# Kernel tuning notes

Hardware: AMD Instinct MI355X
Metric: run time of the kernel (lower is better)

## Reference

```python
import jax, jax.numpy as jnp
import numpy as np

N = 4096   # query tokens
M = 4096   # key/value tokens
D = 512    # embedding_dim


def setup_inputs() -> dict:
    key = jax.random.key(0)
    kq, kk, kv = jax.random.split(key, 3)
    return {
        "query": jax.random.normal(kq, (N, D), dtype=jnp.float32),
        "key": jax.random.normal(kk, (M, D), dtype=jnp.float32),
        "value": jax.random.normal(kv, (M, D), dtype=jnp.float32),
    }


def reference(query, key, value):
    # scores = Q K^T  (no 1/sqrt(d) scaling in the original module)
    attention_scores = jnp.einsum("nd,md->nm", query, key)  # [N, M]
    attention_probs = jax.nn.softmax(attention_scores, axis=-1)  # [N, M]
    output = jnp.einsum("nm,md->nd", attention_probs, value)  # [N, D]
    return (output, attention_probs)
```

## Files before the change

kernel.cpp:

```cpp
#include <hip/hip_runtime.h>
#include <hip/hip_bf16.h>
#include <stdint.h>

#define N_Q 4096
#define N_K 4096
#define DIM 512

typedef float f32x4 __attribute__((ext_vector_type(4)));
typedef __bf16 bf16x8 __attribute__((ext_vector_type(8)));
typedef unsigned short u16x4 __attribute__((ext_vector_type(4)));

__device__ __forceinline__ f32x4 mfma_bf16(bf16x8 a, bf16x8 b, f32x4 c) {
  return __builtin_amdgcn_mfma_f32_16x16x32_bf16(a, b, c, 0, 0, 0);
}

__device__ __forceinline__ void gload16(const void* g, void* l) {
  __builtin_amdgcn_global_load_lds((const __attribute__((address_space(1))) void*)g,
                                   (__attribute__((address_space(3))) void*)l,
                                   16, 0, 0);
}

__device__ __forceinline__ void split4(const f32x4 v, u16x4& h, u16x4& l) {
#pragma unroll
  for (int i = 0; i < 4; ++i) {
    float f = v[i];
    uint32_t u = __builtin_bit_cast(uint32_t, f);
    uint32_t hb = (u + 0x8000u) & 0xffff0000u;
    float hf = __builtin_bit_cast(float, hb);
    float lf = f - hf;
    h[i] = (unsigned short)(hb >> 16);
    l[i] = (unsigned short)(__builtin_bit_cast(uint32_t, lf) >> 16);
  }
}

__device__ __forceinline__ unsigned short bf16r(float f) {
  uint32_t u = __builtin_bit_cast(uint32_t, f);
  return (unsigned short)((u + 0x8000u) >> 16);
}

__global__ __launch_bounds__(256, 2) void qk_kernel(const float* __restrict__ Q,
                                                    const float* __restrict__ K,
                                                    float* __restrict__ S) {
  __shared__ __align__(16) char sAh[16384];
  __shared__ __align__(16) char sAl[16384];
  __shared__ __align__(16) char sBh[16384];
  __shared__ __align__(16) char sBl[16384];

  const int tid = threadIdx.x;
  const int rbase = blockIdx.y * 128;
  const int cbase = blockIdx.x * 128;
  const int lane = tid & 63, wid = tid >> 6;
  const int wr = wid >> 1, wc = wid & 1;
  const int lr = lane & 15, lk = (lane >> 4) * 8;

  const int srow = tid >> 4;
  const int scol = (tid & 15) * 4;

  f32x4 qr[8], kr[8];
#pragma unroll
  for (int p = 0; p < 8; ++p) {
    int r = p * 16 + srow;
    qr[p] = *(const f32x4*)(Q + (size_t)(rbase + r) * DIM + scol);
    kr[p] = *(const f32x4*)(K + (size_t)(cbase + r) * DIM + scol);
  }

  const f32x4 fzero = {0.f, 0.f, 0.f, 0.f};
  f32x4 acc[4][4];
#pragma unroll
  for (int m = 0; m < 4; ++m)
#pragma unroll
    for (int n = 0; n < 4; ++n) acc[m][n] = fzero;

  for (int kk = 0; kk < DIM / 64; ++kk) {
    __syncthreads();
#pragma unroll
    for (int p = 0; p < 8; ++p) {
      int r = p * 16 + srow;
      uint32_t bo = (uint32_t)(r * 128) + (uint32_t)((scol * 2) ^ ((r & 7) << 4));
      u16x4 qh, ql, kh, kl;
      split4(qr[p], qh, ql);
      split4(kr[p], kh, kl);
      *(u16x4*)(sAh + bo) = qh;
      *(u16x4*)(sAl + bo) = ql;
      *(u16x4*)(sBh + bo) = kh;
      *(u16x4*)(sBl + bo) = kl;
    }
    __syncthreads();
    if (kk < DIM / 64 - 1) {
#pragma unroll
      for (int p = 0; p < 8; ++p) {
        int r = p * 16 + srow;
        qr[p] = *(const f32x4*)(Q + (size_t)(rbase + r) * DIM + (kk + 1) * 64 + scol);
        kr[p] = *(const f32x4*)(K + (size_t)(cbase + r) * DIM + (kk + 1) * 64 + scol);
      }
    }
#pragma unroll
    for (int kh = 0; kh < 2; ++kh) {
      bf16x8 a_h[4], a_l[4], b_h[4], b_l[4];
#pragma unroll
      for (int m = 0; m < 4; ++m) {
        int row = wr * 64 + m * 16 + lr;
        uint32_t co = (uint32_t)(((kh * 32 + lk) * 2) ^ ((row & 7) << 4));
        a_h[m] = *(const bf16x8*)(sAh + row * 128 + co);
        a_l[m] = *(const bf16x8*)(sAl + row * 128 + co);
      }
#pragma unroll
      for (int n = 0; n < 4; ++n) {
        int row = wc * 64 + n * 16 + lr;
        uint32_t co = (uint32_t)(((kh * 32 + lk) * 2) ^ ((row & 7) << 4));
        b_h[n] = *(const bf16x8*)(sBh + row * 128 + co);
        b_l[n] = *(const bf16x8*)(sBl + row * 128 + co);
      }
#pragma unroll
      for (int m = 0; m < 4; ++m)
#pragma unroll
        for (int n = 0; n < 4; ++n) {
          acc[m][n] = mfma_bf16(a_h[m], b_h[n], acc[m][n]);
          acc[m][n] = mfma_bf16(a_h[m], b_l[n], acc[m][n]);
          acc[m][n] = mfma_bf16(a_l[m], b_h[n], acc[m][n]);
        }
    }
  }

#pragma unroll
  for (int m = 0; m < 4; ++m) {
    int row = rbase + wr * 64 + m * 16 + (lane >> 4) * 4;
#pragma unroll
    for (int n = 0; n < 4; ++n) {
      int col = cbase + wc * 64 + n * 16 + lr;
#pragma unroll
      for (int j = 0; j < 4; ++j)
        S[(size_t)(row + j) * N_K + col] = acc[m][n][j];
    }
  }
}

__global__ __launch_bounds__(256) void softmax_kernel(float* __restrict__ P,
                                                      unsigned short* __restrict__ Pb) {
  const int tid = threadIdx.x;
  const int wid = tid >> 6, lane = tid & 63;
  float* p = P + (size_t)blockIdx.x * N_K;

  f32x4 v[4];
  float mx = -3.0e38f;
#pragma unroll
  for (int i = 0; i < 4; ++i) {
    v[i] = *(const f32x4*)(p + i * 1024 + tid * 4);
    mx = fmaxf(mx, fmaxf(fmaxf(v[i][0], v[i][1]), fmaxf(v[i][2], v[i][3])));
  }
#pragma unroll
  for (int o = 32; o > 0; o >>= 1) mx = fmaxf(mx, __shfl_xor(mx, o, 64));
  __shared__ float redM[4];
  __shared__ float redS[4];
  if (lane == 0) redM[wid] = mx;
  __syncthreads();
  mx = fmaxf(fmaxf(redM[0], redM[1]), fmaxf(redM[2], redM[3]));

  float s = 0.f;
#pragma unroll
  for (int i = 0; i < 4; ++i) {
#pragma unroll
    for (int j = 0; j < 4; ++j) {
      v[i][j] = __expf(v[i][j] - mx);
      s += v[i][j];
    }
  }
#pragma unroll
  for (int o = 32; o > 0; o >>= 1) s += __shfl_xor(s, o, 64);
  if (lane == 0) redS[wid] = s;
  __syncthreads();
  s = redS[0] + redS[1] + redS[2] + redS[3];
  const float inv = 1.0f / s;

  unsigned short* pb = Pb ? (Pb + (size_t)blockIdx.x * N_K) : nullptr;
#pragma unroll
  for (int i = 0; i < 4; ++i) {
    v[i] *= inv;
    *(f32x4*)(p + i * 1024 + tid * 4) = v[i];
    if (pb) {
      u16x4 h;
#pragma unroll
      for (int j = 0; j < 4; ++j) h[j] = bf16r(v[i][j]);
      *(u16x4*)(pb + i * 1024 + tid * 4) = h;
    }
  }
}

__global__ __launch_bounds__(256) void vt_kernel(const float* __restrict__ V,
                                                 unsigned short* __restrict__ Vt) {
  __shared__ unsigned short t[64][72];
  const int tid = threadIdx.x;
  const int d0 = blockIdx.x * 64;
  const int k0 = blockIdx.y * 64;

#pragma unroll
  for (int c = 0; c < 4; ++c) {
    int kr = (tid >> 4) + c * 16;
    f32x4 v = *(const f32x4*)(V + (size_t)(k0 + kr) * DIM + d0 + (tid & 15) * 4);
#pragma unroll
    for (int j = 0; j < 4; ++j) t[(tid & 15) * 4 + j][kr] = bf16r(v[j]);
  }
  __syncthreads();
#pragma unroll
  for (int c = 0; c < 2; ++c) {
    int d = (tid >> 3) + c * 32;
    int k = (tid & 7) * 8;
    *(uint4*)(Vt + (size_t)(d0 + d) * N_K + k0 + k) = *(const uint4*)&t[d][k];
  }
}

__global__ __launch_bounds__(256, 2) void pv3_kernel(const unsigned short* __restrict__ Pb,
                                                     const unsigned short* __restrict__ Vt,
                                                     float* __restrict__ Opart,
                                                     int kspan) {
  __shared__ __align__(16) char smem[65536];

  const int tid = threadIdx.x;
  const int lane = tid & 63, wid = tid >> 6;
  const int wr = wid >> 1, wc = wid & 1;
  const int rbase = blockIdx.y * 128;
  const int cbase = blockIdx.x * 128;
  const int k0 = blockIdx.z * kspan;
  float* Out = Opart + (size_t)blockIdx.z * ((size_t)N_Q * DIM);

  const int lrow = lane >> 3;
  const int lchk = lane & 7;
  const int iters = kspan >> 6;

  const f32x4 fzero = {0.f, 0.f, 0.f, 0.f};
  f32x4 acc[4][4];
#pragma unroll
  for (int m = 0; m < 4; ++m)
#pragma unroll
    for (int n = 0; n < 4; ++n) acc[m][n] = fzero;

  auto stage = [&](int buf, int t) {
    const size_t kel = (size_t)k0 + ((size_t)t << 6);
#pragma unroll
    for (int i = 0; i < 4; ++i) {
      const int rr = (wid << 5) + (i << 3) + lrow;
      const int gc = lchk ^ (rr & 7);
      const void* gA = (const void*)(Pb + (size_t)(rbase + rr) * N_K + kel + (gc << 3));
      uint32_t off = (uint32_t)(buf * 32768 + (((wid << 5) + (i << 3)) << 7));
      off = (uint32_t)__builtin_amdgcn_readfirstlane((int)off);
      gload16(gA, smem + off);
    }
#pragma unroll
    for (int i = 0; i < 4; ++i) {
      const int rr = (wid << 5) + (i << 3) + lrow;
      const int gc = lchk ^ (rr & 7);
      const void* gB = (const void*)(Vt + (size_t)(cbase + rr) * N_K + kel + (gc << 3));
      uint32_t off = (uint32_t)(buf * 32768 + 16384 + (((wid << 5) + (i << 3)) << 7));
      off = (uint32_t)__builtin_amdgcn_readfirstlane((int)off);
      gload16(gB, smem + off);
    }
  };

  auto compute = [&](int buf) {
    const char* bA = smem + buf * 32768;
    const char* bB = bA + 16384;
#pragma unroll
    for (int kh = 0; kh < 2; ++kh) {
      bf16x8 a[4], b[4];
#pragma unroll
      for (int m = 0; m < 4; ++m) {
        int row = (wr << 6) + (m << 4) + (lane & 15);
        uint32_t co = (uint32_t)(((((kh << 2) + (lane >> 4)) << 4)) ^ ((row & 7) << 4));
        a[m] = *(const bf16x8*)(bA + row * 128 + co);
      }
#pragma unroll
      for (int n = 0; n < 4; ++n) {
        int row = (wc << 6) + (n << 4) + (lane & 15);
        uint32_t co = (uint32_t)(((((kh << 2) + (lane >> 4)) << 4)) ^ ((row & 7) << 4));
        b[n] = *(const bf16x8*)(bB + row * 128 + co);
      }
#pragma unroll
      for (int m = 0; m < 4; ++m)
#pragma unroll
        for (int n = 0; n < 4; ++n)
          acc[m][n] = mfma_bf16(a[m], b[n], acc[m][n]);
    }
  };

  stage(0, 0);
  __syncthreads();
  int cur = 0;
  for (int t = 0; t < iters; ++t) {
    if (t + 1 < iters) stage(cur ^ 1, t + 1);
    compute(cur);
    __syncthreads();
    cur ^= 1;
  }

#pragma unroll
  for (int m = 0; m < 4; ++m) {
    int row = rbase + wr * 64 + m * 16 + (lane >> 4) * 4;
#pragma unroll
    for (int n = 0; n < 4; ++n) {
      int col = cbase + wc * 64 + n * 16 + (lane & 15);
#pragma unroll
      for (int j = 0; j < 4; ++j)
        Out[(size_t)(row + j) * DIM + col] = acc[m][n][j];
    }
  }
}

__global__ __launch_bounds__(256) void reduce_kernel(float* __restrict__ O,
                                                     const float* __restrict__ Opart,
                                                     int nsplit) {
  size_t i = ((size_t)blockIdx.x * 256 + threadIdx.x) * 4;
  f32x4 s = *(const f32x4*)(Opart + i);
  for (int z = 1; z < nsplit; ++z)
    s += *(const f32x4*)(Opart + (size_t)z * ((size_t)N_Q * DIM) + i);
  *(f32x4*)(O + i) = s;
}

__global__ __launch_bounds__(512, 2) void pv_kernel(const float* __restrict__ P,
                                                    const float* __restrict__ V,
                                                    float* __restrict__ O) {
  __shared__ __align__(16) char sA[16384];
  __shared__ __align__(16) char sB[16384];

  const int tid = threadIdx.x;
  const int rbase = blockIdx.y * 128;
  const int cbase = blockIdx.x * 128;
  const int lane = tid & 63, wid = tid >> 6;
  const int wr = wid >> 2, wc = wid & 3;
  const int lr = lane & 15, lk = (lane >> 4) * 8;

  const int a_row = tid >> 4;
  const int a_col = (tid & 15) * 4;
  const int b_c = tid & 127;
  const int b_oct = tid >> 7;

  f32x4 areg[4];
  float breg[4][4];
#pragma unroll
  for (int p = 0; p < 4; ++p) {
    int r = p * 32 + a_row;
    areg[p] = *(const f32x4*)(P + (size_t)(rbase + r) * N_K + a_col);
  }
#pragma unroll
  for (int g = 0; g < 4; ++g) {
    int kr0 = b_oct * 4 + g * 16;
#pragma unroll
    for (int i = 0; i < 4; ++i)
      breg[g][i] = V[(size_t)(kr0 + i) * DIM + cbase + b_c];
  }

  const f32x4 fzero = {0.f, 0.f, 0.f, 0.f};
  f32x4 acc[4][2];
#pragma unroll
  for (int m = 0; m < 4; ++m)
#pragma unroll
    for (int n = 0; n < 2; ++n) acc[m][n] = fzero;

  for (int kk = 0; kk < N_K / 64; ++kk) {
    __syncthreads();
#pragma unroll
    for (int p = 0; p < 4; ++p) {
      int r = p * 32 + a_row;
      uint32_t bo = (uint32_t)(r * 128) + (uint32_t)((a_col * 2) ^ ((r & 7) << 4));
      u16x4 hv;
#pragma unroll
      for (int i = 0; i < 4; ++i) hv[i] = bf16r(areg[p][i]);
      *(u16x4*)(sA + bo) = hv;
    }
#pragma unroll
    for (int g = 0; g < 4; ++g) {
      int kr0 = b_oct * 4 + g * 16;
      uint32_t bo = (uint32_t)(b_c * 128) + (uint32_t)((kr0 * 2) ^ ((b_c & 7) << 4));
      u16x4 hv;
#pragma unroll
      for (int i = 0; i < 4; ++i) hv[i] = bf16r(breg[g][i]);
      *(u16x4*)(sB + bo) = hv;
    }
    __syncthreads();
    if (kk < N_K / 64 - 1) {
#pragma unroll
      for (int p = 0; p < 4; ++p) {
        int r = p * 32 + a_row;
        areg[p] = *(const f32x4*)(P + (size_t)(rbase + r) * N_K + (kk + 1) * 64 + a_col);
      }
#pragma unroll
      for (int g = 0; g < 4; ++g) {
        int kr0 = b_oct * 4 + g * 16;
#pragma unroll
        for (int i = 0; i < 4; ++i)
          breg[g][i] = V[(size_t)((kk + 1) * 64 + kr0 + i) * DIM + cbase + b_c];
      }
    }
#pragma unroll
    for (int kh = 0; kh < 2; ++kh) {
      bf16x8 af[4], bf[2];
#pragma unroll
      for (int m = 0; m < 4; ++m) {
        int row = wr * 64 + m * 16 + lr;
        uint32_t co = (uint32_t)(((kh * 32 + lk) * 2) ^ ((row & 7) << 4));
        af[m] = *(const bf16x8*)(sA + row * 128 + co);
      }
#pragma unroll
      for (int n = 0; n < 2; ++n) {
        int row = wc * 32 + n * 16 + lr;
        uint32_t co = (uint32_t)(((kh * 32 + lk) * 2) ^ ((row & 7) << 4));
        bf[n] = *(const bf16x8*)(sB + row * 128 + co);
      }
#pragma unroll
      for (int m = 0; m < 4; ++m)
#pragma unroll
        for (int n = 0; n < 2; ++n)
          acc[m][n] = mfma_bf16(af[m], bf[n], acc[m][n]);
    }
  }

#pragma unroll
  for (int m = 0; m < 4; ++m) {
    int row = rbase + wr * 64 + m * 16 + (lane >> 4) * 4;
#pragma unroll
    for (int n = 0; n < 2; ++n) {
      int col = cbase + wc * 32 + n * 16 + lr;
#pragma unroll
      for (int j = 0; j < 4; ++j)
        O[(size_t)(row + j) * DIM + col] = acc[m][n][j];
    }
  }
}

extern "C" void kernel_launch(void* const* d_in, const int* in_sizes, int n_in,
                              void* d_out, int out_size, void* d_ws, size_t ws_size,
                              hipStream_t stream) {
  const float* Q = (const float*)d_in[0];
  const float* K = (const float*)d_in[1];
  const float* V = (const float*)d_in[2];
  float* O = (float*)d_out;
  float* P = O + (size_t)N_Q * DIM;

  const size_t PB_BYTES = (size_t)N_Q * N_K * 2;
  const size_t VT_BYTES = (size_t)DIM * N_K * 2;
  const size_t OP_BYTES = (size_t)N_Q * DIM * 4;

  int nsplit = 0;
  if (ws_size >= PB_BYTES + VT_BYTES + 4 * OP_BYTES) nsplit = 4;
  else if (ws_size >= PB_BYTES + VT_BYTES + 2 * OP_BYTES) nsplit = 2;
  else if (ws_size >= PB_BYTES + VT_BYTES) nsplit = 1;

  qk_kernel<<<dim3(N_K / 128, N_Q / 128), 256, 0, stream>>>(Q, K, P);

  if (nsplit > 0) {
    unsigned short* Pb = (unsigned short*)d_ws;
    unsigned short* Vt = (unsigned short*)((char*)d_ws + PB_BYTES);
    float* Opart = (float*)((char*)d_ws + PB_BYTES + VT_BYTES);

    vt_kernel<<<dim3(DIM / 64, N_K / 64), 256, 0, stream>>>(V, Vt);
    softmax_kernel<<<N_Q, 256, 0, stream>>>(P, Pb);
    if (nsplit == 1) {
      pv3_kernel<<<dim3(DIM / 128, N_Q / 128, 1), 256, 0, stream>>>(Pb, Vt, O, N_K);
    } else {
      pv3_kernel<<<dim3(DIM / 128, N_Q / 128, nsplit), 256, 0, stream>>>(Pb, Vt, Opart, N_K / nsplit);
      reduce_kernel<<<(N_Q * DIM) / (256 * 4), 256, 0, stream>>>(O, Opart, nsplit);
    }
  } else {
    softmax_kernel<<<N_Q, 256, 0, stream>>>(P, nullptr);
    pv_kernel<<<dim3(DIM / 128, N_Q / 128), 512, 0, stream>>>(P, V, O);
  }
}
```

Before: 124.3 us.

## Pre-split Q and K into bf16 hi/lo planes before the QK GEMM

```diff
diff --git a/kernel.cpp b/kernel.cpp
--- a/kernel.cpp
+++ b/kernel.cpp
@@ -9,6 +9,7 @@
 typedef float f32x4 __attribute__((ext_vector_type(4)));
 typedef __bf16 bf16x8 __attribute__((ext_vector_type(8)));
 typedef unsigned short u16x4 __attribute__((ext_vector_type(4)));
+typedef unsigned short u16x8 __attribute__((ext_vector_type(8)));
 
 __device__ __forceinline__ f32x4 mfma_bf16(bf16x8 a, bf16x8 b, f32x4 c) {
   return __builtin_amdgcn_mfma_f32_16x16x32_bf16(a, b, c, 0, 0, 0);
@@ -36,6 +37,124 @@
 __device__ __forceinline__ unsigned short bf16r(float f) {
   uint32_t u = __builtin_bit_cast(uint32_t, f);
   return (unsigned short)((u + 0x8000u) >> 16);
+}
+
+__global__ __launch_bounds__(256) void split_kernel(const float* __restrict__ X,
+                                                    unsigned short* __restrict__ X2) {
+  const size_t base = ((size_t)blockIdx.x * 256 + threadIdx.x) * 8;
+  const size_t row = base >> 9;
+  const size_t col = base & 511;
+  u16x8 H, L;
+#pragma unroll
+  for (int h = 0; h < 2; ++h) {
+    f32x4 v = *(const f32x4*)(X + base + h * 4);
+    u16x4 hh, ll;
+    split4(v, hh, ll);
+#pragma unroll
+    for (int j = 0; j < 4; ++j) { H[h * 4 + j] = hh[j]; L[h * 4 + j] = ll[j]; }
+  }
+  *(u16x8*)(X2 + row * 1024 + col) = H;
+  *(u16x8*)(X2 + row * 1024 + 512 + col) = L;
+}
+
+__global__ __launch_bounds__(256, 2) void qk2_kernel(const unsigned short* __restrict__ Xq,
+                                                     const unsigned short* __restrict__ Xk,
+                                                     float* __restrict__ S) {
+  __shared__ __align__(16) char smem[65536];
+
+  const int tid = threadIdx.x;
+  const int lane = tid & 63, wid = tid >> 6;
+  const int wr = wid >> 1, wc = wid & 1;
+
+  const int bid = blockIdx.x;
+  const int b = (bid & 7) * 128 + (bid >> 3);
+  const int rbase = (b >> 5) * 128;
+  const int cbase = (b & 31) * 128;
+
+  const int lrow = lane >> 3;
+  const int lchk = lane & 7;
+
+  const f32x4 fzero = {0.f, 0.f, 0.f, 0.f};
+  f32x4 acc[4][4];
+#pragma unroll
+  for (int m = 0; m < 4; ++m)
+#pragma unroll
+    for (int n = 0; n < 4; ++n) acc[m][n] = fzero;
+
+  auto stage = [&](int buf, int t) {
+#pragma unroll
+    for (int i = 0; i < 4; ++i) {
+      const int r = (wid << 5) + (i << 3) + lrow;
+      const int sc = lchk ^ (r & 7);
+      const unsigned short* g =
+          Xq + (size_t)(rbase + r) * 1024 + (sc >> 2) * 512 + t * 32 + (sc & 3) * 8;
+      uint32_t off = (uint32_t)(buf * 32768 + (((wid << 5) + (i << 3)) << 7));
+      off = (uint32_t)__builtin_amdgcn_readfirstlane((int)off);
+      gload16(g, smem + off);
+    }
+#pragma unroll
+    for (int i = 0; i < 4; ++i) {
+      const int r = (wid << 5) + (i << 3) + lrow;
+      const int sc = lchk ^ (r & 7);
+      const unsigned short* g =
+          Xk + (size_t)(cbase + r) * 1024 + (sc >> 2) * 512 + t * 32 + (sc & 3) * 8;
+      uint32_t off = (uint32_t)(buf * 32768 + 16384 + (((wid << 5) + (i << 3)) << 7));
+      off = (uint32_t)__builtin_amdgcn_readfirstlane((int)off);
+      gload16(g, smem + off);
+    }
+  };
+
+  auto compute = [&](int buf) {
+    const char* bA = smem + buf * 32768;
+    const char* bB = bA + 16384;
+    bf16x8 ah[4], al[4], bh[4], bl[4];
+#pragma unroll
+    for (int m = 0; m < 4; ++m) {
+      int row = (wr << 6) + (m << 4) + (lane & 15);
+      int ch = (lane >> 4) ^ (row & 7);
+      int cl = (4 + (lane >> 4)) ^ (row & 7);
+      ah[m] = *(const bf16x8*)(bA + row * 128 + ch * 16);
+      al[m] = *(const bf16x8*)(bA + row * 128 + cl * 16);
+    }
+#pragma unroll
+    for (int n = 0; n < 4; ++n) {
+      int row = (wc << 6) + (n << 4) + (lane & 15);
+      int ch = (lane >> 4) ^ (row & 7);
+      int cl = (4 + (lane >> 4)) ^ (row & 7);
+      bh[n] = *(const bf16x8*)(bB + row * 128 + ch * 16);
+      bl[n] = *(const bf16x8*)(bB + row * 128 + cl * 16);
+    }
+#pragma unroll
+    for (int m = 0; m < 4; ++m)
+#pragma unroll
+      for (int n = 0; n < 4; ++n) {
+        acc[m][n] = mfma_bf16(ah[m], bh[n], acc[m][n]);
+        acc[m][n] = mfma_bf16(ah[m], bl[n], acc[m][n]);
+        acc[m][n] = mfma_bf16(al[m], bh[n], acc[m][n]);
+      }
+  };
+
+  stage(0, 0);
+  __syncthreads();
+  int cur = 0;
+  for (int t = 0; t < 16; ++t) {
+    if (t + 1 < 16) stage(cur ^ 1, t + 1);
+    compute(cur);
+    __syncthreads();
+    cur ^= 1;
+  }
+
+#pragma unroll
+  for (int m = 0; m < 4; ++m) {
+    int row = rbase + wr * 64 + m * 16 + (lane >> 4) * 4;
+#pragma unroll
+    for (int n = 0; n < 4; ++n) {
+      int col = cbase + wc * 64 + n * 16 + (lane & 15);
+#pragma unroll
+      for (int j = 0; j < 4; ++j)
+        S[(size_t)(row + j) * N_K + col] = acc[m][n][j];
+    }
+  }
 }
 
 __global__ __launch_bounds__(256, 2) void qk_kernel(const float* __restrict__ Q,
@@ -444,14 +563,17 @@
   else if (ws_size >= PB_BYTES + VT_BYTES + 2 * OP_BYTES) nsplit = 2;
   else if (ws_size >= PB_BYTES + VT_BYTES) nsplit = 1;
 
-  qk_kernel<<<dim3(N_K / 128, N_Q / 128), 256, 0, stream>>>(Q, K, P);
-
   if (nsplit > 0) {
+    unsigned short* Xq = (unsigned short*)d_ws;
+    unsigned short* Xk = Xq + (size_t)N_Q * 1024;
     unsigned short* Pb = (unsigned short*)d_ws;
     unsigned short* Vt = (unsigned short*)((char*)d_ws + PB_BYTES);
     float* Opart = (float*)((char*)d_ws + PB_BYTES + VT_BYTES);
 
+    split_kernel<<<1024, 256, 0, stream>>>(Q, Xq);
+    split_kernel<<<1024, 256, 0, stream>>>(K, Xk);
     vt_kernel<<<dim3(DIM / 64, N_K / 64), 256, 0, stream>>>(V, Vt);
+    qk2_kernel<<<1024, 256, 0, stream>>>(Xq, Xk, P);
     softmax_kernel<<<N_Q, 256, 0, stream>>>(P, Pb);
     if (nsplit == 1) {
       pv3_kernel<<<dim3(DIM / 128, N_Q / 128, 1), 256, 0, stream>>>(Pb, Vt, O, N_K);
@@ -460,6 +582,7 @@
       reduce_kernel<<<(N_Q * DIM) / (256 * 4), 256, 0, stream>>>(O, Opart, nsplit);
     }
   } else {
+    qk_kernel<<<dim3(N_K / 128, N_Q / 128), 256, 0, stream>>>(Q, K, P);
     softmax_kernel<<<N_Q, 256, 0, stream>>>(P, nullptr);
     pv_kernel<<<dim3(DIM / 128, N_Q / 128), 512, 0, stream>>>(P, V, O);
   }
```

After: 131.4 us. +5.6%, slower.
